# Kernel optimization log

Measured on AMD Instinct MI355X. Metric: run time of the kernel, lower is better.

Reference implementation:

```python
import jax, jax.numpy as jnp
import numpy as np

B, T, D, F, E, K = 4, 2048, 1024, 2048, 8, 2


def setup_inputs() -> dict:
    key = jax.random.key(0)
    ks = jax.random.split(key, 5)
    s = lambda n: 1.0 / np.sqrt(n)
    return {
        "x": jax.random.normal(ks[0], (B, T, D), jnp.float32),
        "gate_w": jax.random.normal(ks[1], (D, E), jnp.float32) * s(D),
        "gate_b": jnp.zeros((E,), jnp.float32),
        "w1": jax.random.normal(ks[2], (E, D, F), jnp.float32) * s(D),
        "b1": jnp.zeros((E, F), jnp.float32),
        "w2": jax.random.normal(ks[3], (E, F, D), jnp.float32) * s(F),
        "b2": jnp.zeros((E, D), jnp.float32),
    }


def reference(x, gate_w, gate_b, w1, b1, w2, b2):
    # Router: gate logits -> top-k -> softmax over the k selected logits
    logits = x @ gate_w + gate_b                      # [B,T,E]
    top_v, top_i = jax.lax.top_k(logits, K)           # [B,T,K]
    top_w = jax.nn.softmax(top_v, axis=-1)            # [B,T,K]
    # Dense combine weights per expert: w_full[b,t,e] = sum_k top_w * 1[top_i==e]
    one_hot = jax.nn.one_hot(top_i, E, dtype=x.dtype)  # [B,T,K,E]
    w_full = jnp.sum(top_w[..., None] * one_hot, axis=-2)  # [B,T,E]
    # All-experts FFN (batched over expert dim), exact-erf GELU as in nn.GELU()
    h = jax.nn.gelu(jnp.einsum('btd,edf->ebtf', x, w1) + b1[:, None, None, :],
                    approximate=False)                 # [E,B,T,F]
    y = jnp.einsum('ebtf,efd->ebtd', h, w2) + b2[:, None, None, :]  # [E,B,T,D]
    # Weighted combine (zero weight for unselected experts == masked dispatch)
    return jnp.einsum('bte,ebtd->btd', w_full, y)      # [B,T,D]
```

## Files before the change

### kernel.cpp

```cpp
#include <hip/hip_runtime.h>
#include <hip/hip_bf16.h>
#include <math.h>

#define B_ 4
#define T_ 2048
#define D_ 1024
#define F_ 2048
#define E_ 8
#define NT (B_ * T_)
#define NS (NT * 2)
#define CAP (NS + E_ * 128)

typedef __attribute__((ext_vector_type(8))) short short8;
typedef __attribute__((ext_vector_type(4))) float floatx4;

static __device__ __forceinline__ unsigned short f2bf(float f) {
  union { float f; unsigned u; } a; a.f = f;
  unsigned r = a.u + 0x7fffu + ((a.u >> 16) & 1u);
  return (unsigned short)(r >> 16);
}

static __device__ __forceinline__ float bf2f(unsigned u) {
  union { unsigned u; float f; } a; a.u = u << 16; return a.f;
}

static __device__ __forceinline__ void gld16(const unsigned short* g, unsigned short* l) {
  __builtin_amdgcn_global_load_lds(
      (const __attribute__((address_space(1))) void*)g,
      (__attribute__((address_space(3))) void*)l, 16, 0, 0);
}

static __device__ __forceinline__ float gelu_f(float v) {
  float ax = fabsf(v) * 0.70710678118654752f;
  float t = __builtin_amdgcn_rcpf(1.f + 0.3275911f * ax);
  float e = __builtin_amdgcn_exp2f(-ax * ax * 1.44269504088896f);
  float p = t * (0.254829592f +
            t * (-0.284496736f +
            t * (1.421413741f +
            t * (-1.453152027f +
            t * 1.061405429f))));
  float er = 1.f - p * e;
  er = copysignf(er, v);
  return 0.5f * v * (1.f + er);
}

__global__ void transpose_cvt(const float* __restrict__ in, unsigned short* __restrict__ out,
                              int R, int C) {
  __shared__ float tile[32][33];
  int e = blockIdx.z;
  const float* inp = in + (size_t)e * R * C;
  unsigned short* outp = out + (size_t)e * R * C;
  int c0 = blockIdx.x * 32, r0 = blockIdx.y * 32;
  int tx = threadIdx.x, ty = threadIdx.y;
#pragma unroll
  for (int j = 0; j < 4; j++)
    tile[ty + 8 * j][tx] = inp[(size_t)(r0 + ty + 8 * j) * C + c0 + tx];
  __syncthreads();
#pragma unroll
  for (int j = 0; j < 4; j++)
    outp[(size_t)(c0 + ty + 8 * j) * R + r0 + tx] = f2bf(tile[tx][ty + 8 * j]);
}

__global__ void router_k(const float* __restrict__ x, const float* __restrict__ gw,
                         const float* __restrict__ gb, int* __restrict__ ti,
                         float* __restrict__ tw) {
  int wid = threadIdx.x >> 6, lane = threadIdx.x & 63;
  int t = blockIdx.x * 4 + wid;
  const float* xr = x + (size_t)t * D_;
  float acc[E_];
#pragma unroll
  for (int e = 0; e < E_; e++) acc[e] = 0.f;
#pragma unroll
  for (int it = 0; it < D_ / 64; it++) {
    int d = it * 64 + lane;
    float xv = xr[d];
    const float* g = gw + d * E_;
#pragma unroll
    for (int e = 0; e < E_; e++) acc[e] += xv * g[e];
  }
#pragma unroll
  for (int off = 32; off > 0; off >>= 1)
#pragma unroll
    for (int e = 0; e < E_; e++) acc[e] += __shfl_xor(acc[e], off);
  if (lane == 0) {
    float v[E_];
#pragma unroll
    for (int e = 0; e < E_; e++) v[e] = acc[e] + gb[e];
    int i0 = 0; float v0 = v[0];
#pragma unroll
    for (int e = 1; e < E_; e++) if (v[e] > v0) { v0 = v[e]; i0 = e; }
    int i1 = -1; float v1 = -3.4e38f;
#pragma unroll
    for (int e = 0; e < E_; e++) if (e != i0 && v[e] > v1) { v1 = v[e]; i1 = e; }
    float ex = expf(v1 - v0);
    float w0 = 1.f / (1.f + ex);
    float w1 = ex / (1.f + ex);
    ti[2 * t] = i0; tw[2 * t] = w0;
    ti[2 * t + 1] = i1; tw[2 * t + 1] = w1;
  }
}

__global__ void count_prefix_k(const int* __restrict__ ti, int* __restrict__ offs,
                               int* __restrict__ cursors) {
  __shared__ int scnt[4][E_];
  int tid = threadIdx.x;
  int cnt[E_];
#pragma unroll
  for (int k = 0; k < E_; k++) cnt[k] = 0;
  for (int i = tid; i < NS; i += 256) {
    int e = ti[i];
#pragma unroll
    for (int k = 0; k < E_; k++) cnt[k] += (e == k) ? 1 : 0;
  }
#pragma unroll
  for (int off = 32; off > 0; off >>= 1)
#pragma unroll
    for (int k = 0; k < E_; k++) cnt[k] += __shfl_xor(cnt[k], off);
  int wid = tid >> 6, lane = tid & 63;
  if (lane == 0)
#pragma unroll
    for (int k = 0; k < E_; k++) scnt[wid][k] = cnt[k];
  __syncthreads();
  if (tid == 0) {
    int o = 0;
    for (int k = 0; k < E_; k++) {
      int c = scnt[0][k] + scnt[1][k] + scnt[2][k] + scnt[3][k];
      offs[k] = o;
      cursors[k] = o;
      o += (c + 127) & ~127;
    }
    offs[E_] = o;
  }
}

__global__ void scatter_k(const int* __restrict__ ti, const float* __restrict__ tw,
                          int* __restrict__ cursors, int* __restrict__ idx,
                          int* __restrict__ pos_of) {
  int a = blockIdx.x * 256 + threadIdx.x;
  int lane = threadIdx.x & 63;
  int e = ti[a];
  unsigned long long m[E_];
#pragma unroll
  for (int k = 0; k < E_; k++) m[k] = __ballot(e == k);
  int base = 0;
  if (lane < E_) base = atomicAdd(&cursors[lane], __popcll(m[lane]));
  int myBase = __shfl(base, e);
  unsigned long long m_mine = 0;
#pragma unroll
  for (int k = 0; k < E_; k++) if (e == k) m_mine = m[k];
  int rank = __popcll(m_mine & ((1ull << lane) - 1ull));
  int pos = myBase + rank;
  idx[pos] = a >> 1;
  pos_of[a] = pos;
}

__global__ void gather_k(const float* __restrict__ x, const int* __restrict__ idx,
                         unsigned short* __restrict__ Xg) {
  int s = blockIdx.x;
  int t = idx[s];
  t = ((unsigned)t < (unsigned)NT) ? t : 0;
  const float4* xr = (const float4*)(x + (size_t)t * D_);
  float4 v = xr[threadIdx.x];
  uint2 p;
  p.x = (unsigned)f2bf(v.x) | ((unsigned)f2bf(v.y) << 16);
  p.y = (unsigned)f2bf(v.z) | ((unsigned)f2bf(v.w) << 16);
  ((uint2*)(Xg + (size_t)s * D_))[threadIdx.x] = p;
}

template <int K, int N, bool GELU>
__global__ __launch_bounds__(256, 3) void gemm_k(const unsigned short* __restrict__ A,
                                                 const unsigned short* __restrict__ W,
                                                 const float* __restrict__ bias_all,
                                                 unsigned short* __restrict__ O,
                                                 const int* __restrict__ offs) {
  int slot0 = blockIdx.y * 128;
  if (slot0 >= offs[E_]) return;
  int e = 0;
  while (slot0 >= offs[e + 1]) e++;
  const unsigned short* Bp = W + (size_t)e * N * K;
  int n0 = blockIdx.x * 128;

  __shared__ unsigned short lA[3][128 * 32];
  __shared__ unsigned short lB[3][128 * 32];

  int tid = threadIdx.x;
  int wid = tid >> 6, lane = tid & 63;
  int wr = wid >> 1, wc = wid & 1;
  int quad = lane >> 4, l15 = lane & 15;

  int cph = (((l15 & 1) << 2) | quad) ^ ((l15 >> 1) & 7);
  int ra = ((wr << 5) + (l15 >> 1)) * 64 + cph * 8;
  int rb = ((wc << 5) + (l15 >> 1)) * 64 + cph * 8;

  int srl = lane >> 3;
  int clog = (lane & 7) ^ srl;
  int r_l = (srl << 1) | (clog >> 2);
  int q_l = clog & 3;
  const unsigned short* gA = A + (size_t)(slot0 + 32 * wid + r_l) * K + q_l * 8;
  const unsigned short* gB = Bp + (size_t)(n0 + 32 * wid + r_l) * K + q_l * 8;

#define STG(buf, kt) do {                                                \
    gld16(gA + (size_t)(kt) * 32, &lA[buf][(32 * wid) * 32]);            \
    gld16(gA + (size_t)16 * K + (size_t)(kt) * 32,                       \
          &lA[buf][(32 * wid + 16) * 32]);                               \
    gld16(gB + (size_t)(kt) * 32, &lB[buf][(32 * wid) * 32]);            \
    gld16(gB + (size_t)16 * K + (size_t)(kt) * 32,                       \
          &lB[buf][(32 * wid + 16) * 32]);                               \
  } while (0)
#define SYNC4 asm volatile("s_waitcnt vmcnt(4)\n\ts_barrier" ::: "memory")

  floatx4 acc[4][4];
#pragma unroll
  for (int mi = 0; mi < 4; mi++)
#pragma unroll
    for (int ni = 0; ni < 4; ni++) acc[mi][ni] = (floatx4){0.f, 0.f, 0.f, 0.f};

  constexpr int NK = K / 32;

  STG(0, 0);
  STG(1, 1);
  SYNC4;

#define STEP(j, t) do {                                                  \
    int kt = ((t) + 2 < NK) ? (t) + 2 : 0;                               \
    STG(((j) + 2) % 3, kt);                                              \
    short8 af[4], bfr[4];                                                \
    _Pragma("unroll")                                                    \
    for (int m = 0; m < 4; m++) af[m] = *(const short8*)&lA[j][ra + m * 512]; \
    _Pragma("unroll")                                                    \
    for (int n = 0; n < 4; n++) bfr[n] = *(const short8*)&lB[j][rb + n * 512]; \
    _Pragma("unroll")                                                    \
    for (int m = 0; m < 4; m++)                                          \
      _Pragma("unroll")                                                  \
      for (int n = 0; n < 4; n++)                                        \
        acc[m][n] = __builtin_amdgcn_mfma_f32_16x16x32_bf16(af[m], bfr[n], acc[m][n], 0, 0, 0); \
    SYNC4;                                                               \
  } while (0)

  for (int t3 = 0; t3 < NK; t3 += 3) {
    STEP(0, t3);
    if (t3 + 1 < NK) STEP(1, t3 + 1);
    if (t3 + 2 < NK) STEP(2, t3 + 2);
  }
#undef STEP
#undef STG
#undef SYNC4

  const float* bias = bias_all + (size_t)e * N;
#pragma unroll
  for (int mi = 0; mi < 4; mi++) {
    int row = slot0 + 64 * wr + 16 * mi + quad * 4;
#pragma unroll
    for (int ni = 0; ni < 4; ni++) {
      int col = n0 + 64 * wc + 16 * ni + l15;
      float bv = bias[col];
#pragma unroll
      for (int r = 0; r < 4; r++) {
        float v = acc[mi][ni][r] + bv;
        if (GELU) v = gelu_f(v);
        O[(size_t)(row + r) * N + col] = f2bf(v);
      }
    }
  }
}

__global__ void combine_k(const unsigned short* __restrict__ Yg,
                          const int* __restrict__ pos_of,
                          const float* __restrict__ tw, float* __restrict__ out) {
  int t = blockIdx.x;
  int p0 = pos_of[2 * t], p1 = pos_of[2 * t + 1];
  float w0 = tw[2 * t], w1 = tw[2 * t + 1];
  uint2 a = ((const uint2*)(Yg + (size_t)p0 * D_))[threadIdx.x];
  uint2 b = ((const uint2*)(Yg + (size_t)p1 * D_))[threadIdx.x];
  float4 r;
  r.x = w0 * bf2f(a.x & 0xffffu) + w1 * bf2f(b.x & 0xffffu);
  r.y = w0 * bf2f(a.x >> 16)     + w1 * bf2f(b.x >> 16);
  r.z = w0 * bf2f(a.y & 0xffffu) + w1 * bf2f(b.y & 0xffffu);
  r.w = w0 * bf2f(a.y >> 16)     + w1 * bf2f(b.y >> 16);
  ((float4*)(out + (size_t)t * D_))[threadIdx.x] = r;
}

extern "C" void kernel_launch(void* const* d_in, const int* in_sizes, int n_in,
                              void* d_out, int out_size, void* d_ws, size_t ws_size,
                              hipStream_t stream) {
  const float* x  = (const float*)d_in[0];
  const float* gw = (const float*)d_in[1];
  const float* gb = (const float*)d_in[2];
  const float* w1 = (const float*)d_in[3];
  const float* b1 = (const float*)d_in[4];
  const float* w2 = (const float*)d_in[5];
  const float* b2 = (const float*)d_in[6];
  float* out = (float*)d_out;

  char* p = (char*)d_ws;
  unsigned short* w1t = (unsigned short*)p; p += (size_t)E_ * D_ * F_ * 2;
  unsigned short* w2t = (unsigned short*)p; p += (size_t)E_ * D_ * F_ * 2;
  unsigned short* Xg  = (unsigned short*)p; p += (size_t)CAP * D_ * 2;
  unsigned short* H   = (unsigned short*)p; p += (size_t)CAP * F_ * 2;
  int*   idx    = (int*)p; p += (size_t)CAP * 4;
  int*   pos_of = (int*)p; p += (size_t)NS * 4;
  int*   ti     = (int*)p; p += (size_t)NS * 4;
  float* tw     = (float*)p; p += (size_t)NS * 4;
  int* cursors = (int*)p; p += 64;
  int* offs    = (int*)p; p += 64;
  unsigned short* Yg = Xg;

  dim3 tb(32, 8);
  transpose_cvt<<<dim3(F_ / 32, D_ / 32, E_), tb, 0, stream>>>(w1, w1t, D_, F_);
  transpose_cvt<<<dim3(D_ / 32, F_ / 32, E_), tb, 0, stream>>>(w2, w2t, F_, D_);
  router_k<<<NT / 4, 256, 0, stream>>>(x, gw, gb, ti, tw);
  count_prefix_k<<<1, 256, 0, stream>>>(ti, offs, cursors);
  scatter_k<<<NS / 256, 256, 0, stream>>>(ti, tw, cursors, idx, pos_of);
  gather_k<<<CAP, 256, 0, stream>>>(x, idx, Xg);
  gemm_k<D_, F_, true><<<dim3(F_ / 128, CAP / 128), 256, 0, stream>>>(Xg, w1t, b1, H, offs);
  gemm_k<F_, D_, false><<<dim3(D_ / 128, CAP / 128), 256, 0, stream>>>(H, w2t, b2, Yg, offs);
  combine_k<<<NT, 256, 0, stream>>>(Yg, pos_of, tw, out);
}
```

Before: 484.2 us.

## Vectorize weight transpose with 64x64 tiles and remap GEMM blocks across XCDs

The weight transpose/convert kernel now uses 64x64 tiles, float4 global loads and 16-byte packed bf16 stores instead of scalar accesses, to cut memory transaction count. The GEMM kernels switch to a 1D grid whose block index is permuted so that consecutive logical tiles land on the same XCD (round-robin of 8), which should improve L2 reuse of A rows and weight tiles. The LDS tile with 65-float padding may still see some bank conflicts on the strided column reads, and the remap assumes the grid size is divisible by 8.

```diff
diff --git a/kernel.cpp b/kernel.cpp
--- a/kernel.cpp
+++ b/kernel.cpp
@@ -46,19 +46,36 @@
 
 __global__ void transpose_cvt(const float* __restrict__ in, unsigned short* __restrict__ out,
                               int R, int C) {
-  __shared__ float tile[32][33];
+  __shared__ float tile[64][65];
   int e = blockIdx.z;
   const float* inp = in + (size_t)e * R * C;
   unsigned short* outp = out + (size_t)e * R * C;
-  int c0 = blockIdx.x * 32, r0 = blockIdx.y * 32;
-  int tx = threadIdx.x, ty = threadIdx.y;
-#pragma unroll
-  for (int j = 0; j < 4; j++)
-    tile[ty + 8 * j][tx] = inp[(size_t)(r0 + ty + 8 * j) * C + c0 + tx];
+  int c0 = blockIdx.x * 64, r0 = blockIdx.y * 64;
+  int tid = threadIdx.x;
+  int rl = tid >> 4;
+  int cl = (tid & 15) * 4;
+#pragma unroll
+  for (int jr = 0; jr < 4; jr++) {
+    int row = rl + 16 * jr;
+    float4 v = *(const float4*)&inp[(size_t)(r0 + row) * C + c0 + cl];
+    tile[row][cl + 0] = v.x; tile[row][cl + 1] = v.y;
+    tile[row][cl + 2] = v.z; tile[row][cl + 3] = v.w;
+  }
   __syncthreads();
-#pragma unroll
-  for (int j = 0; j < 4; j++)
-    outp[(size_t)(c0 + ty + 8 * j) * R + r0 + tx] = f2bf(tile[tx][ty + 8 * j]);
+  int cc0 = tid >> 3;
+  int rq = (tid & 7) * 8;
+#pragma unroll
+  for (int jc = 0; jc < 2; jc++) {
+    int cc = cc0 + 32 * jc;
+    unsigned w[4];
+#pragma unroll
+    for (int i = 0; i < 4; i++) {
+      unsigned lo = f2bf(tile[rq + 2 * i][cc]);
+      unsigned hi = f2bf(tile[rq + 2 * i + 1][cc]);
+      w[i] = lo | (hi << 16);
+    }
+    *(uint4*)&outp[(size_t)(c0 + cc) * R + r0 + rq] = make_uint4(w[0], w[1], w[2], w[3]);
+  }
 }
 
 __global__ void router_k(const float* __restrict__ x, const float* __restrict__ gw,
@@ -173,12 +190,16 @@
                                                  const float* __restrict__ bias_all,
                                                  unsigned short* __restrict__ O,
                                                  const int* __restrict__ offs) {
-  int slot0 = blockIdx.y * 128;
+  constexpr int NC = N / 128;
+  int h = blockIdx.x;
+  int logical = (h & 7) * ((int)gridDim.x >> 3) + (h >> 3);
+  int rt = logical / NC, ct = logical - rt * NC;
+  int slot0 = rt * 128;
   if (slot0 >= offs[E_]) return;
   int e = 0;
   while (slot0 >= offs[e + 1]) e++;
   const unsigned short* Bp = W + (size_t)e * N * K;
-  int n0 = blockIdx.x * 128;
+  int n0 = ct * 128;
 
   __shared__ unsigned short lA[3][128 * 32];
   __shared__ unsigned short lB[3][128 * 32];
@@ -305,14 +326,13 @@
   int* offs    = (int*)p; p += 64;
   unsigned short* Yg = Xg;
 
-  dim3 tb(32, 8);
-  transpose_cvt<<<dim3(F_ / 32, D_ / 32, E_), tb, 0, stream>>>(w1, w1t, D_, F_);
-  transpose_cvt<<<dim3(D_ / 32, F_ / 32, E_), tb, 0, stream>>>(w2, w2t, F_, D_);
+  transpose_cvt<<<dim3(F_ / 64, D_ / 64, E_), 256, 0, stream>>>(w1, w1t, D_, F_);
+  transpose_cvt<<<dim3(D_ / 64, F_ / 64, E_), 256, 0, stream>>>(w2, w2t, F_, D_);
   router_k<<<NT / 4, 256, 0, stream>>>(x, gw, gb, ti, tw);
   count_prefix_k<<<1, 256, 0, stream>>>(ti, offs, cursors);
   scatter_k<<<NS / 256, 256, 0, stream>>>(ti, tw, cursors, idx, pos_of);
   gather_k<<<CAP, 256, 0, stream>>>(x, idx, Xg);
-  gemm_k<D_, F_, true><<<dim3(F_ / 128, CAP / 128), 256, 0, stream>>>(Xg, w1t, b1, H, offs);
-  gemm_k<F_, D_, false><<<dim3(D_ / 128, CAP / 128), 256, 0, stream>>>(H, w2t, b2, Yg, offs);
+  gemm_k<D_, F_, true><<<dim3((CAP / 128) * (F_ / 128)), 256, 0, stream>>>(Xg, w1t, b1, H, offs);
+  gemm_k<F_, D_, false><<<dim3((CAP / 128) * (D_ / 128)), 256, 0, stream>>>(H, w2t, b2, Yg, offs);
   combine_k<<<NT, 256, 0, stream>>>(Yg, pos_of, tw, out);
 }
```

New measurement: 465.0 us. -3.9%, faster.
